# Kernel tuning notes

Hardware: AMD Instinct MI355X
Metric: run time of the kernel (lower is better)

The kernel has to match this reference:

```python
import jax, jax.numpy as jnp
import numpy as np

# Model constants (from module __init__ / repo script)
DT = 60                    # model time step [s]
DT_FORCING = 3600          # forcing time step [s]
NSUB = DT_FORCING // DT    # substeps between forcing samples = 60
NT = 5_040_000             # number of model steps (~9.6 years at dt=60s)
NF = NT // NSUB            # forcing series length = 84000
FC = 1e-4                  # Coriolis frequency


def setup_inputs() -> dict:
    key = jax.random.key(0)
    k1, k2, k3 = jax.random.split(key, 3)
    # pk = log(K); K ~ exp(-10) ~ 4.5e-5 keeps the Euler recurrence stable (|a|<1)
    pk = -10.0 + 0.1 * jax.random.normal(k1, (2,), dtype=jnp.float32)
    # wind stress forcing, around the repo's 0.2 N/m^2 zonal value
    TAx = 0.2 + 0.05 * jax.random.normal(k2, (NF,), dtype=jnp.float32)
    TAy = 0.05 * jax.random.normal(k3, (NF,), dtype=jnp.float32)
    return {"pk": pk, "TAx": TAx, "TAy": TAy}


def reference(pk, TAx, TAy):
    K = jnp.exp(pk)                                    # K[0]: wind coeff, K[1]: damping
    TA = TAx.astype(jnp.complex64) + 1j * TAy.astype(jnp.complex64)  # [NF]

    # Vectorized linear interpolation of forcing onto every model step it=0..NT-2
    it = jnp.arange(NT - 1)
    itf = it // NSUB
    aa = (it % NSUB).astype(jnp.float32) / NSUB
    # faithful to original: compares against NT (never true), then relies on
    # JAX's clamping gather for the final out-of-range itf+1
    itsup = jnp.where(itf + 1 >= NT, -1, itf + 1)
    TAi = (1.0 - aa) * TA[itf] + aa * TA[itsup]        # [NT-1] complex64

    # U_{t+1} = U_t + dt*(-i*fc*U_t + K0*TA_t - K1*U_t) = a*U_t + b_t
    a = jnp.asarray(1.0 + DT * (-1j * FC - K[1]), dtype=jnp.complex64)
    b = (DT * K[0]).astype(jnp.complex64) * TAi        # [NT-1]

    def step(u, bt):
        u_next = a * u + bt
        return u_next, u_next

    u0 = jnp.zeros((), dtype=jnp.complex64)
    _, ys = jax.lax.scan(step, u0, b)                  # [NT-1]
    U = jnp.concatenate([u0[None], ys])                # [NT], U[0] = 0
    return jnp.real(U), jnp.imag(U)
```

## Files before the change

### kernel.cpp

```cpp
#include <hip/hip_runtime.h>
#include <math.h>

#define NTOT   5040000
#define NFORC  84000
#define NSTEPS (NTOT - 1)

#define TPB    256
#define SEGS   60
#define WIN    (TPB * SEGS)
#define WARM   4800
#define CHUNK  (WIN - WARM)
#define NBLK   ((NSTEPS + CHUNK - 1) / CHUNK)

struct cd { double x, y; };
__device__ __forceinline__ cd cmuld(cd a, cd b){ return {a.x*b.x - a.y*b.y, a.x*b.y + a.y*b.x}; }
__device__ __forceinline__ cd cdivd(cd a, cd b){
    double r = 1.0 / (b.x*b.x + b.y*b.y);
    return {(a.x*b.x + a.y*b.y)*r, (a.y*b.x - a.x*b.y)*r};
}
__device__ __forceinline__ cd cpowd(cd a, int e){
    cd r = {1.0, 0.0}; cd p = a;
    while (e) { if (e & 1) r = cmuld(r, p); p = cmuld(p, p); e >>= 1; }
    return r;
}

__device__ __forceinline__ float2 cfma(float2 m, float2 p, float2 v) {
    v.x = fmaf(m.x, p.x, fmaf(-m.y, p.y, v.x));
    v.y = fmaf(m.x, p.y, fmaf( m.y, p.x, v.y));
    return v;
}
__device__ __forceinline__ float2 cmulf(float2 a, float2 b){
    return make_float2(a.x*b.x - a.y*b.y, a.x*b.y + a.y*b.x);
}

__global__ __launch_bounds__(TPB, 4)
void slab_kernel(const float* __restrict__ pk,
                 const float* __restrict__ TAx,
                 const float* __restrict__ TAy,
                 float* __restrict__ out)
{
    __shared__ float2 sA[SEGS], sG[SEGS], sH[SEGS];
    __shared__ float2 sU0[TPB], sB0[TPB], sDB[TPB];
    __shared__ float2 wk[4];

    const int tid  = threadIdx.x;
    const int lane = tid & 63;
    const int wv   = tid >> 6;
    const int blk  = blockIdx.x;

    const double K0 = exp((double)pk[0]);
    const double K1 = exp((double)pk[1]);
    const cd a   = {1.0 - 60.0 * K1, -60.0e-4};
    const double s = 60.0 * K0;
    const cd am1     = {a.x - 1.0, a.y};
    const cd one_m_a = {-am1.x, -am1.y};
    const cd om2     = cmuld(one_m_a, one_m_a);

    const cd alpha = cpowd(a, SEGS);
    const cd G60 = cdivd({alpha.x - 1.0, alpha.y}, am1);
    const cd a59 = cdivd(alpha, a);
    cd num60 = {1.0 - 60.0*a59.x + 59.0*alpha.x, -60.0*a59.y + 59.0*alpha.y};
    const cd T60 = cdivd(cmuld(a, num60), om2);
    const cd H60 = {59.0*G60.x - T60.x, 59.0*G60.y - T60.y};

    const float2 Gf = make_float2((float)G60.x, (float)G60.y);
    const float2 Hf = make_float2((float)H60.x, (float)H60.y);
    float2 apf[6]; float2 betaf;
    {
        cd p = alpha;
        #pragma unroll
        for (int k = 0; k < 6; ++k) { apf[k] = make_float2((float)p.x, (float)p.y); p = cmuld(p, p); }
        betaf = make_float2((float)p.x, (float)p.y);
    }

    if (tid < SEGS) {
        const int j = tid + 1;
        const cd aj = cpowd(a, j);
        const cd Gj = cdivd({aj.x - 1.0, aj.y}, am1);
        const cd ajm1 = cdivd(aj, a);
        cd nm = {1.0 - (double)j*ajm1.x + (double)(j-1)*aj.x,
                      - (double)j*ajm1.y + (double)(j-1)*aj.y};
        const cd Tj = cdivd(cmuld(a, nm), om2);
        const cd Hj = {(double)(j-1)*Gj.x - Tj.x, (double)(j-1)*Gj.y - Tj.y};
        sA[tid] = make_float2((float)aj.x, (float)aj.y);
        sG[tid] = make_float2((float)Gj.x, (float)Gj.y);
        sH[tid] = make_float2((float)Hj.x, (float)Hj.y);
    }

    const int wstart = blk * CHUNK;
    const int wend   = min(wstart + CHUNK, NSTEPS);
    const int ws     = max(0, wstart - WARM);

    const int itf = ws / SEGS + tid;
    const int i0  = min(itf,     NFORC - 1);
    const int i1  = min(itf + 1, NFORC - 1);
    const float x0 = TAx[i0], y0 = TAy[i0];
    const float x1 = TAx[i1], y1 = TAy[i1];
    const float sF = (float)s;
    const float2 b0 = make_float2(sF * x0, sF * y0);
    const float  ci = sF * (1.0f / 60.0f);
    const float2 db = make_float2((x1 - x0) * ci, (y1 - y0) * ci);
    sB0[tid] = b0;
    sDB[tid] = db;

    float2 S = cfma(Gf, b0, cmulf(Hf, db));

    #pragma unroll
    for (int k = 0; k < 6; ++k) {
        const int off = 1 << k;
        float px = __shfl_up(S.x, off, 64);
        float py = __shfl_up(S.y, off, 64);
        if (lane < off) { px = 0.f; py = 0.f; }
        S = cfma(apf[k], make_float2(px, py), S);
    }
    float ex = __shfl_up(S.x, 1, 64);
    float ey = __shfl_up(S.y, 1, 64);
    if (lane == 0) { ex = 0.f; ey = 0.f; }

    if (lane == 63) wk[wv] = S;
    __syncthreads();
    float2 C = make_float2(0.f, 0.f);
    if (wv >= 1) C = wk[0];
    if (wv >= 2) C = cfma(betaf, C, wk[1]);
    if (wv == 3) C = cfma(betaf, C, wk[2]);

    float2 al = make_float2(1.f, 0.f);
    #pragma unroll
    for (int k = 0; k < 6; ++k)
        if (lane & (1 << k)) al = cmulf(al, apf[k]);

    const float2 u0 = cfma(al, C, make_float2(ex, ey));
    sU0[tid] = u0;
    __syncthreads();

    if (blk == 0 && tid == 0) { out[0] = 0.f; out[NTOT] = 0.f; }

    const int qlo = wstart + 1;
    const int qhi = wend + 1;
    const int g0  = qlo & ~3;
    const int ng  = (qhi - g0 + 3) >> 2;

    for (int k = tid; k < ng; k += TPB) {
        const int q4 = g0 + (k << 2);
        float re[4], im[4];
        #pragma unroll
        for (int e = 0; e < 4; ++e) {
            const int q = q4 + e;
            if (q < qlo || q >= qhi) { re[e] = 0.f; im[e] = 0.f; continue; }
            const int m   = q - 1 - ws;
            const int seg = (int)((unsigned)m / 60u);
            const int r   = m - seg * 60;
            const float2 A  = sA[r];
            const float2 Gv = sG[r];
            const float2 Hv = sH[r];
            float2 u = cmulf(A, sU0[seg]);
            u = cfma(Gv, sB0[seg], u);
            u = cfma(Hv, sDB[seg], u);
            re[e] = u.x; im[e] = u.y;
        }
        if (q4 >= qlo && q4 + 4 <= qhi) {
            *reinterpret_cast<float4*>(out + q4)        = make_float4(re[0], re[1], re[2], re[3]);
            *reinterpret_cast<float4*>(out + NTOT + q4) = make_float4(im[0], im[1], im[2], im[3]);
        } else {
            #pragma unroll
            for (int e = 0; e < 4; ++e) {
                const int q = q4 + e;
                if (q >= qlo && q < qhi) { out[q] = re[e]; out[NTOT + q] = im[e]; }
            }
        }
    }
}

extern "C" void kernel_launch(void* const* d_in, const int* in_sizes, int n_in,
                              void* d_out, int out_size, void* d_ws, size_t ws_size,
                              hipStream_t stream)
{
    const float* pk  = (const float*)d_in[0];
    const float* TAx = (const float*)d_in[1];
    const float* TAy = (const float*)d_in[2];
    float* out = (float*)d_out;

    slab_kernel<<<dim3(NBLK), dim3(TPB), 0, stream>>>(pk, TAx, TAy, out);
}
```

Baseline: 80.80 us.

## Replace per-element closed-form evaluation with per-thread serial recurrence staged through LDS

Instead of evaluating each output from precomputed A/G/H power tables (three complex FMAs per element plus table lookups), each thread now runs the 60-step recurrence serially from its segment start value, writing results into a padded LDS tile. The tile is then streamed to global memory with coalesced scalar stores. Only one wave computes at a time, in four phases separated by barriers, which serializes compute and adds syncs. The float4 vector stores are replaced by scalar stores, and the float32 serial recurrence may accumulate slightly more rounding error.

```diff
diff --git a/kernel.cpp b/kernel.cpp
--- a/kernel.cpp
+++ b/kernel.cpp
@@ -11,6 +11,9 @@
 #define WARM   4800
 #define CHUNK  (WIN - WARM)
 #define NBLK   ((NSTEPS + CHUNK - 1) / CHUNK)
+#define RSEG   64
+#define RSPAN  (RSEG * SEGS)
+#define LSTR   61
 
 struct cd { double x, y; };
 __device__ __forceinline__ cd cmuld(cd a, cd b){ return {a.x*b.x - a.y*b.y, a.x*b.y + a.y*b.x}; }
@@ -39,8 +42,8 @@
                  const float* __restrict__ TAy,
                  float* __restrict__ out)
 {
-    __shared__ float2 sA[SEGS], sG[SEGS], sH[SEGS];
-    __shared__ float2 sU0[TPB], sB0[TPB], sDB[TPB];
+    __shared__ float  sRe[RSEG * LSTR];
+    __shared__ float  sIm[RSEG * LSTR];
     __shared__ float2 wk[4];
 
     const int tid  = threadIdx.x;
@@ -72,20 +75,8 @@
         for (int k = 0; k < 6; ++k) { apf[k] = make_float2((float)p.x, (float)p.y); p = cmuld(p, p); }
         betaf = make_float2((float)p.x, (float)p.y);
     }
-
-    if (tid < SEGS) {
-        const int j = tid + 1;
-        const cd aj = cpowd(a, j);
-        const cd Gj = cdivd({aj.x - 1.0, aj.y}, am1);
-        const cd ajm1 = cdivd(aj, a);
-        cd nm = {1.0 - (double)j*ajm1.x + (double)(j-1)*aj.x,
-                      - (double)j*ajm1.y + (double)(j-1)*aj.y};
-        const cd Tj = cdivd(cmuld(a, nm), om2);
-        const cd Hj = {(double)(j-1)*Gj.x - Tj.x, (double)(j-1)*Gj.y - Tj.y};
-        sA[tid] = make_float2((float)aj.x, (float)aj.y);
-        sG[tid] = make_float2((float)Gj.x, (float)Gj.y);
-        sH[tid] = make_float2((float)Hj.x, (float)Hj.y);
-    }
+    const float arf = (float)a.x;
+    const float aif = (float)a.y;
 
     const int wstart = blk * CHUNK;
     const int wend   = min(wstart + CHUNK, NSTEPS);
@@ -100,8 +91,6 @@
     const float2 b0 = make_float2(sF * x0, sF * y0);
     const float  ci = sF * (1.0f / 60.0f);
     const float2 db = make_float2((x1 - x0) * ci, (y1 - y0) * ci);
-    sB0[tid] = b0;
-    sDB[tid] = db;
 
     float2 S = cfma(Gf, b0, cmulf(Hf, db));
 
@@ -130,44 +119,48 @@
         if (lane & (1 << k)) al = cmulf(al, apf[k]);
 
     const float2 u0 = cfma(al, C, make_float2(ex, ey));
-    sU0[tid] = u0;
-    __syncthreads();
 
     if (blk == 0 && tid == 0) { out[0] = 0.f; out[NTOT] = 0.f; }
 
-    const int qlo = wstart + 1;
-    const int qhi = wend + 1;
-    const int g0  = qlo & ~3;
-    const int ng  = (qhi - g0 + 3) >> 2;
+    const int olo = wstart - ws;
+    const int ohi = wend - ws;
 
-    for (int k = tid; k < ng; k += TPB) {
-        const int q4 = g0 + (k << 2);
-        float re[4], im[4];
-        #pragma unroll
-        for (int e = 0; e < 4; ++e) {
-            const int q = q4 + e;
-            if (q < qlo || q >= qhi) { re[e] = 0.f; im[e] = 0.f; continue; }
-            const int m   = q - 1 - ws;
-            const int seg = (int)((unsigned)m / 60u);
-            const int r   = m - seg * 60;
-            const float2 A  = sA[r];
-            const float2 Gv = sG[r];
-            const float2 Hv = sH[r];
-            float2 u = cmulf(A, sU0[seg]);
-            u = cfma(Gv, sB0[seg], u);
-            u = cfma(Hv, sDB[seg], u);
-            re[e] = u.x; im[e] = u.y;
-        }
-        if (q4 >= qlo && q4 + 4 <= qhi) {
-            *reinterpret_cast<float4*>(out + q4)        = make_float4(re[0], re[1], re[2], re[3]);
-            *reinterpret_cast<float4*>(out + NTOT + q4) = make_float4(im[0], im[1], im[2], im[3]);
-        } else {
+    for (int p = 0; p < 4; ++p) {
+        const int lo = max(RSPAN * p, olo);
+        const int hi = min(RSPAN * p + RSPAN, ohi);
+        if (hi <= lo) continue;
+
+        if (wv == p) {
+            float ur = u0.x, ui = u0.y;
+            float bre = b0.x, bim = b0.y;
+            const int base = lane * LSTR;
             #pragma unroll
-            for (int e = 0; e < 4; ++e) {
-                const int q = q4 + e;
-                if (q >= qlo && q < qhi) { out[q] = re[e]; out[NTOT + q] = im[e]; }
+            for (int r = 0; r < SEGS; ++r) {
+                float nr = fmaf(arf, ur, fmaf(-aif, ui, bre));
+                float ni = fmaf(arf, ui, fmaf( aif, ur, bim));
+                ur = nr; ui = ni;
+                bre += db.x; bim += db.y;
+                sRe[base + r] = nr;
+                sIm[base + r] = ni;
             }
         }
+        __syncthreads();
+
+        {
+            int rel = lo + tid - RSPAN * p;
+            int sseg = (int)((unsigned)rel / 60u);
+            int k    = rel - sseg * 60;
+            float* __restrict__ pr = out + (ws + 1);
+            float* __restrict__ pi = out + (NTOT + ws + 1);
+            for (int idx = lo + tid; idx < hi; idx += TPB) {
+                const int addr = LSTR * sseg + k;
+                pr[idx] = sRe[addr];
+                pi[idx] = sIm[addr];
+                sseg += 4; k += 16;
+                if (k >= SEGS) { k -= SEGS; sseg += 1; }
+            }
+        }
+        __syncthreads();
     }
 }
 
```

Result: faster. 78.55 us (-2.8%).
